# Optimization experiments

Measured on AMD Instinct MI355X. Metric: run time of the kernel, lower is better.

## Reference

```python
import jax, jax.numpy as jnp
import numpy as np
from jax import lax

N_LAYER = 24
N_EMBD = 1024
FFN = 4 * N_EMBD
LN_EPS = 1e-5


def setup_inputs() -> dict:
    key = jax.random.key(0)
    ks = jax.random.split(key, 24)
    L, C, F = N_LAYER, N_EMBD, FFN
    s = C ** -0.5  # keep GEMV outputs O(1) so exp() stays finite

    def rn(k, shape, scale=1.0):
        return jax.random.normal(k, shape, dtype=jnp.float32) * scale

    state = jnp.concatenate([
        rn(ks[1], (1, L, C)),                                          # statea: prev ln1 output
        rn(ks[2], (1, L, C), 0.1),                                     # stateb: wkv numerator acc
        jax.random.uniform(ks[3], (1, L, C), dtype=jnp.float32) + 0.5, # statec: wkv denominator acc (>0)
        rn(ks[4], (1, L, C)),                                          # stated: prev ln2 output
    ], axis=0)

    return {
        "x": rn(ks[0], (C,)),
        "state": state,
        "ln1w": 1.0 + rn(ks[5], (L, C), 0.02),
        "ln1b": rn(ks[6], (L, C), 0.02),
        "ln2w": 1.0 + rn(ks[7], (L, C), 0.02),
        "ln2b": rn(ks[8], (L, C), 0.02),
        "time_decay": -jnp.abs(rn(ks[9], (L, C))) - 0.1,
        "time_first": rn(ks[10], (L, C), 0.1),
        "kktk": jax.random.uniform(ks[11], (L, C), dtype=jnp.float32),
        "vvtv": jax.random.uniform(ks[12], (L, C), dtype=jnp.float32),
        "rrtr": jax.random.uniform(ks[13], (L, C), dtype=jnp.float32),
        "key": rn(ks[14], (L, 3, C, C), s),        # [kk, vv, -rr] stacks
        "outputv": rn(ks[15], (L, C, C), s),
        "time_mix_k_ffn": jax.random.uniform(ks[16], (L, C), dtype=jnp.float32),
        "time_mix_r_ffn": jax.random.uniform(ks[17], (L, C), dtype=jnp.float32),
        "key_ffn": rn(ks[18], (L, F, C), s),
        "receptance_ffn": rn(ks[19], (L, C, C), s),  # stored pre-negated, as in the module
        "value_ffn": rn(ks[20], (L, C, F), F ** -0.5),
    }


def _ln(v, w, b):
    m = v.mean()
    var = ((v - m) ** 2).mean()
    return (v - m) * lax.rsqrt(var + LN_EPS) * w + b


def reference(x, state, ln1w, ln1b, ln2w, ln2b, time_decay, time_first,
              kktk, vvtv, rrtr, key, outputv, time_mix_k_ffn, time_mix_r_ffn,
              key_ffn, receptance_ffn, value_ffn):
    # offset = 0, so the state slice covers all layers
    statea, stateb, statec, stated = state[0], state[1], state[2], state[3]  # each [L, C]
    # token-shift contributions precomputed against previous-step state
    kk_s = kktk * statea
    vv_s = vvtv * statea
    rr_s = rrtr * statea
    tmk_s = time_mix_k_ffn * stated
    tmr_s = time_mix_r_ffn * stated

    def layer(xc, p):
        (l1w, l1b, l2w, l2b, td, tfst, kks, vvs, rrs, keym, outv,
         tmk, tmr, kffn, rffn, vffn, sb, sc) = p
        xy = _ln(xc, l1w, l1b)
        k = keym[0] @ (xy + kks)
        v = keym[1] @ (xy + vvs)
        r = keym[2] @ (xy + rrs)   # keym[2] holds -receptance weights
        etfk = jnp.exp(tfst + k)
        w = (sb + etfk * v) / (sc * jnp.exp(r) + jnp.exp(tfst + k + r) + sc + etfk)
        sxx = xc + outv @ w
        ek = jnp.exp(k)
        ed = jnp.exp(td)
        sb_new = sb * ed + ek * v
        sc_new = sc * ed + ek
        xx = _ln(sxx, l2w, l2b)
        kf = jnp.square(jax.nn.relu(kffn @ (xx + tmk)))
        rf = jnp.exp(rffn @ (xx + tmr))  # rffn already negated
        x_new = sxx + (vffn @ kf) / (rf + 1.0)
        return x_new, (xy, sb_new, sc_new, xx)

    xs = (ln1w, ln1b, ln2w, ln2b, time_decay, time_first, kk_s, vv_s, rr_s,
          key, outputv, tmk_s, tmr_s, key_ffn, receptance_ffn, value_ffn,
          stateb, statec)
    x_out, (sa_n, sb_n, sc_n, sd_n) = lax.scan(layer, x, xs)
    new_state = jnp.stack([sa_n, sb_n, sc_n, sd_n])  # [4, L, C]
    return x_out, new_state
```

## Files before the change

### kernel.cpp

```cpp
#include <hip/hip_runtime.h>
#include <math.h>
#include <stddef.h>

#define NLAYER 24
#define NEMBD  1024
#define NFFN   4096
#define NB     256
#define NT     256
#define LN_EPS 1e-5f

#define OUT_SA (NEMBD)
#define OUT_SB (NEMBD + NLAYER*NEMBD)
#define OUT_SC (NEMBD + 2*NLAYER*NEMBD)
#define OUT_SD (NEMBD + 3*NLAYER*NEMBD)

typedef unsigned long long u64;
typedef unsigned u32;

#define QX_OFF    0
#define QKVR_OFF  1024
#define QSXX_OFF  4096
#define QKFB_OFF  5120
#define QTOTAL    9216

struct Params {
  const float *x, *state, *ln1w, *ln1b, *ln2w, *ln2b, *td, *tf, *kktk, *vvtv, *rrtr;
  const float *key, *outputv, *tmk, *tmr, *kffn, *rffn, *vffn;
  float *out;
  u64 *q;
};

__device__ __forceinline__ float wred(float v) {
#pragma unroll
  for (int o = 32; o > 0; o >>= 1) v += __shfl_xor(v, o, 64);
  return v;
}
__device__ __forceinline__ float dot4(float4 a, float4 b) {
  return a.x*b.x + a.y*b.y + a.z*b.z + a.w*b.w;
}
__device__ __forceinline__ float fcomp(float4 v, int j) {
  return j == 0 ? v.x : (j == 1 ? v.y : (j == 2 ? v.z : v.w));
}
__device__ __forceinline__ u64 qload(const u64* a) {
  return __hip_atomic_load(a, __ATOMIC_RELAXED, __HIP_MEMORY_SCOPE_AGENT);
}
__device__ __forceinline__ void qput(u64* a, float v, u32 tag) {
  u64 w = ((u64)tag << 32) | (u64)__float_as_uint(v);
  __hip_atomic_store(a, w, __ATOMIC_RELAXED, __HIP_MEMORY_SCOPE_AGENT);
}
__device__ __forceinline__ u32   qtag(u64 w) { return (u32)(w >> 32); }
__device__ __forceinline__ float qval(u64 w) { return __uint_as_float((u32)w); }

__device__ __forceinline__ void lbar() {
  asm volatile("s_waitcnt lgkmcnt(0)" ::: "memory");
  __builtin_amdgcn_s_barrier();
  asm volatile("" ::: "memory");
}

__global__ void __launch_bounds__(NT, 1)
rwkv_persistent(Params p) {
  const int b    = blockIdx.x;
  const int t    = threadIdx.x;
  const int wid  = t >> 6;
  const int lane = t & 63;
  const int i0   = t * 4;
  const int rowq = b * 4 + wid;

  __shared__ float lds[NFFN];
  __shared__ float part[8];
  __shared__ float sxw[4];
  __shared__ float rfw[4];

  u64* QX   = p.q + QX_OFF;
  u64* QKVR = p.q + QKVR_OFF;
  u64* QSXX = p.q + QSXX_OFF;
  u64* QKFB = p.q + QKFB_OFF;

  float4 wr[20];

  auto pf1 = [&](int L) {
    const float* W = p.key + (size_t)L * 3 * NEMBD * NEMBD
                   + (size_t)(b * 12 + wid * 3) * NEMBD + lane * 4;
#pragma unroll
    for (int r = 0; r < 3; ++r)
#pragma unroll
      for (int jj = 0; jj < 4; ++jj)
        wr[r * 4 + jj] = *(const float4*)&W[(size_t)r * NEMBD + jj * 256];
  };
  auto pf2 = [&](int L) {
    const float* W = p.outputv + ((size_t)L * NEMBD + rowq) * NEMBD + lane * 4;
#pragma unroll
    for (int jj = 0; jj < 4; ++jj)
      wr[jj] = *(const float4*)&W[jj * 256];
  };
  int isk3[5], rid3[5], voff3[5];
#pragma unroll
  for (int sI = 0; sI < 5; ++sI) {
    int qI = wid * 5 + sI;
    if (qI < 16) { isk3[sI] = 1; rid3[sI] = b * 16 + qI;       voff3[sI] = 0; }
    else         { isk3[sI] = 0; rid3[sI] = b * 4 + (qI - 16); voff3[sI] = NEMBD; }
  }
  auto pf3 = [&](int L) {
#pragma unroll
    for (int sI = 0; sI < 5; ++sI) {
      const float* wp = isk3[sI]
        ? p.kffn + ((size_t)L * NFFN  + rid3[sI]) * NEMBD
        : p.rffn + ((size_t)L * NEMBD + rid3[sI]) * NEMBD;
      wp += lane * 4;
#pragma unroll
      for (int jj = 0; jj < 4; ++jj)
        wr[sI * 4 + jj] = *(const float4*)&wp[jj * 256];
    }
  };
  auto pf4 = [&](int L) {
    const float* W = p.vffn + ((size_t)L * NEMBD + rowq) * NFFN + lane * 4;
#pragma unroll
    for (int jj = 0; jj < 16; ++jj)
      wr[jj] = *(const float4*)&W[jj * 256];
  };

  pf1(0);

  for (int l = 0; l < NLAYER; ++l) {
    const u32 t1 = (u32)(4 * l + 1), t2 = t1 + 1, t3 = t1 + 2, t4 = t1 + 3;
    const bool w1 = (b == (l * 4 + 0) % NB);
    const bool w2 = (b == (l * 4 + 1) % NB);
    const bool w3 = (b == (l * 4 + 2) % NB);

    {
      float xa[4];
      if (l == 0) {
        float4 x4 = *(const float4*)&p.x[i0];
        xa[0] = x4.x; xa[1] = x4.y; xa[2] = x4.z; xa[3] = x4.w;
      } else {
        const u32 tp = (u32)(4 * l);
        u64 a0, a1, a2, a3; long c = 0;
        for (;;) {
          a0 = qload(&QX[i0 + 0]); a1 = qload(&QX[i0 + 1]);
          a2 = qload(&QX[i0 + 2]); a3 = qload(&QX[i0 + 3]);
          if (qtag(a0) >= tp && qtag(a1) >= tp && qtag(a2) >= tp && qtag(a3) >= tp) break;
          __builtin_amdgcn_s_sleep(1);
          if (++c > (1L << 20)) break;
        }
        xa[0] = qval(a0); xa[1] = qval(a1); xa[2] = qval(a2); xa[3] = qval(a3);
      }
      float s = xa[0] + xa[1] + xa[2] + xa[3];
      float q = xa[0]*xa[0] + xa[1]*xa[1] + xa[2]*xa[2] + xa[3]*xa[3];
      s = wred(s); q = wred(q);
      if (lane == 0) { part[wid] = s; part[4 + wid] = q; }
      lbar();
      float m  = (part[0] + part[1] + part[2] + part[3]) * (1.f / NEMBD);
      float tq = (part[4] + part[5] + part[6] + part[7]) * (1.f / NEMBD);
      float rs = rsqrtf(tq - m * m + LN_EPS);
      const int o = l * NEMBD + i0;
      float4 l1w = *(const float4*)&p.ln1w[o];
      float4 l1b = *(const float4*)&p.ln1b[o];
      float4 sa  = *(const float4*)&p.state[0 * NLAYER * NEMBD + o];
      float4 kk  = *(const float4*)&p.kktk[o];
      float4 vv  = *(const float4*)&p.vvtv[o];
      float4 rr  = *(const float4*)&p.rrtr[o];
#pragma unroll
      for (int j = 0; j < 4; ++j) {
        int i = i0 + j;
        float xy  = (xa[j] - m) * rs * fcomp(l1w, j) + fcomp(l1b, j);
        float sav = fcomp(sa, j);
        lds[i]             = xy + fcomp(kk, j) * sav;
        lds[NEMBD + i]     = xy + fcomp(vv, j) * sav;
        lds[2 * NEMBD + i] = xy + fcomp(rr, j) * sav;
        if (w1) p.out[OUT_SA + l * NEMBD + i] = xy;
      }
      lbar();
      const int r0 = b * 12 + wid * 3;
      const float* v0 = lds + ((r0 + 0) >> 10) * NEMBD;
      const float* v1 = lds + ((r0 + 1) >> 10) * NEMBD;
      const float* v2 = lds + ((r0 + 2) >> 10) * NEMBD;
      float a0 = 0.f, a1 = 0.f, a2 = 0.f;
#pragma unroll
      for (int jj = 0; jj < 4; ++jj) {
        int col = lane * 4 + jj * 256;
        a0 += dot4(wr[0 * 4 + jj], *(const float4*)&v0[col]);
        a1 += dot4(wr[1 * 4 + jj], *(const float4*)&v1[col]);
        a2 += dot4(wr[2 * 4 + jj], *(const float4*)&v2[col]);
      }
      a0 = wred(a0); a1 = wred(a1); a2 = wred(a2);
      if (lane == 0) {
        qput(&QKVR[r0 + 0], a0, t1);
        qput(&QKVR[r0 + 1], a1, t1);
        qput(&QKVR[r0 + 2], a2, t1);
      }
      pf2(l);
      lbar();
    }

    {
      float kk[4], vv[4], rv[4];
      {
        u64 wk[4], wv[4], wq[4]; long c = 0;
        for (;;) {
          bool ok = true;
#pragma unroll
          for (int j = 0; j < 4; ++j) {
            wk[j] = qload(&QKVR[i0 + j]);
            wv[j] = qload(&QKVR[NEMBD + i0 + j]);
            wq[j] = qload(&QKVR[2 * NEMBD + i0 + j]);
            ok &= (qtag(wk[j]) >= t1) & (qtag(wv[j]) >= t1) & (qtag(wq[j]) >= t1);
          }
          if (ok) break;
          __builtin_amdgcn_s_sleep(1);
          if (++c > (1L << 20)) break;
        }
#pragma unroll
        for (int j = 0; j < 4; ++j) { kk[j] = qval(wk[j]); vv[j] = qval(wv[j]); rv[j] = qval(wq[j]); }
      }
      float xc;
      if (l == 0) xc = p.x[rowq];
      else {
        const u32 tp = (u32)(4 * l);
        u64 wx; long c = 0;
        for (;;) {
          wx = qload(&QX[rowq]);
          if (qtag(wx) >= tp) break;
          __builtin_amdgcn_s_sleep(1);
          if (++c > (1L << 20)) break;
        }
        xc = qval(wx);
      }
      const int o = l * NEMBD + i0;
      float4 tf = *(const float4*)&p.tf[o];
      float4 sb4 = *(const float4*)&p.state[1 * NLAYER * NEMBD + o];
      float4 sc4 = *(const float4*)&p.state[2 * NLAYER * NEMBD + o];
      float4 td4 = *(const float4*)&p.td[o];
#pragma unroll
      for (int j = 0; j < 4; ++j) {
        float sb = fcomp(sb4, j), sc = fcomp(sc4, j);
        float etfk = expf(fcomp(tf, j) + kk[j]);
        float er   = expf(rv[j]);
        lds[i0 + j] = (sb + etfk * vv[j]) / ((sc + etfk) * (1.f + er));
        if (w2) {
          float ek = expf(kk[j]), ed = expf(fcomp(td4, j));
          p.out[OUT_SB + l * NEMBD + i0 + j] = sb * ed + ek * vv[j];
          p.out[OUT_SC + l * NEMBD + i0 + j] = sc * ed + ek;
        }
      }
      lbar();
      float acc = 0.f;
#pragma unroll
      for (int jj = 0; jj < 4; ++jj) {
        int col = lane * 4 + jj * 256;
        acc += dot4(wr[jj], *(const float4*)&lds[col]);
      }
      acc = wred(acc);
      if (lane == 0) {
        float sxx = xc + acc;
        qput(&QSXX[rowq], sxx, t2);
        sxw[wid] = sxx;
      }
      pf3(l);
      lbar();
    }

    {
      float xa[4];
      {
        u64 a0, a1, a2, a3; long c = 0;
        for (;;) {
          a0 = qload(&QSXX[i0 + 0]); a1 = qload(&QSXX[i0 + 1]);
          a2 = qload(&QSXX[i0 + 2]); a3 = qload(&QSXX[i0 + 3]);
          if (qtag(a0) >= t2 && qtag(a1) >= t2 && qtag(a2) >= t2 && qtag(a3) >= t2) break;
          __builtin_amdgcn_s_sleep(1);
          if (++c > (1L << 20)) break;
        }
        xa[0] = qval(a0); xa[1] = qval(a1); xa[2] = qval(a2); xa[3] = qval(a3);
      }
      float s = xa[0] + xa[1] + xa[2] + xa[3];
      float q = xa[0]*xa[0] + xa[1]*xa[1] + xa[2]*xa[2] + xa[3]*xa[3];
      s = wred(s); q = wred(q);
      if (lane == 0) { part[wid] = s; part[4 + wid] = q; }
      lbar();
      float m  = (part[0] + part[1] + part[2] + part[3]) * (1.f / NEMBD);
      float tq = (part[4] + part[5] + part[6] + part[7]) * (1.f / NEMBD);
      float rs = rsqrtf(tq - m * m + LN_EPS);
      const int o = l * NEMBD + i0;
      float4 l2w = *(const float4*)&p.ln2w[o];
      float4 l2b = *(const float4*)&p.ln2b[o];
      float4 sd4 = *(const float4*)&p.state[3 * NLAYER * NEMBD + o];
      float4 tmk = *(const float4*)&p.tmk[o];
      float4 tmr = *(const float4*)&p.tmr[o];
#pragma unroll
      for (int j = 0; j < 4; ++j) {
        int i = i0 + j;
        float xx  = (xa[j] - m) * rs * fcomp(l2w, j) + fcomp(l2b, j);
        float sdv = fcomp(sd4, j);
        lds[i]         = xx + fcomp(tmk, j) * sdv;
        lds[NEMBD + i] = xx + fcomp(tmr, j) * sdv;
        if (w3) p.out[OUT_SD + l * NEMBD + i] = xx;
      }
      lbar();
      float acc[5] = {0.f, 0.f, 0.f, 0.f, 0.f};
#pragma unroll
      for (int jj = 0; jj < 4; ++jj) {
        int col = lane * 4 + jj * 256;
#pragma unroll
        for (int sI = 0; sI < 5; ++sI)
          acc[sI] += dot4(wr[sI * 4 + jj], *(const float4*)&lds[voff3[sI] + col]);
      }
#pragma unroll
      for (int sI = 0; sI < 5; ++sI) {
        float r = wred(acc[sI]);
        if (lane == 0) {
          if (isk3[sI]) { float kv = fmaxf(r, 0.f); qput(&QKFB[rid3[sI]], kv * kv, t3); }
          else          { rfw[rid3[sI] - b * 4] = expf(r); }
        }
      }
      pf4(l);
      lbar();
    }

    {
      {
        u64 w[16]; long c = 0;
        for (;;) {
          bool ok = true;
#pragma unroll
          for (int pass = 0; pass < 4; ++pass)
#pragma unroll
            for (int j = 0; j < 4; ++j) {
              w[pass * 4 + j] = qload(&QKFB[pass * NEMBD + i0 + j]);
              ok &= (qtag(w[pass * 4 + j]) >= t3);
            }
          if (ok) break;
          __builtin_amdgcn_s_sleep(1);
          if (++c > (1L << 20)) break;
        }
#pragma unroll
        for (int pass = 0; pass < 4; ++pass)
#pragma unroll
          for (int j = 0; j < 4; ++j)
            lds[pass * NEMBD + i0 + j] = qval(w[pass * 4 + j]);
      }
      lbar();
      float accA = 0.f, accB = 0.f;
#pragma unroll
      for (int jj = 0; jj < 16; jj += 2) {
        int col = lane * 4 + jj * 256;
        accA += dot4(wr[jj],     *(const float4*)&lds[col]);
        accB += dot4(wr[jj + 1], *(const float4*)&lds[col + 256]);
      }
      float acc = wred(accA + accB);
      if (lane == 0) {
        float xn = sxw[wid] + acc / (rfw[wid] + 1.f);
        if (l == NLAYER - 1) p.out[rowq] = xn;
        else                 qput(&QX[rowq], xn, t4);
      }
      if (l < NLAYER - 1) pf1(l + 1);
      lbar();
    }
  }
}

__global__ void rwkv_init(u64* q) {
  for (int i = 0; i < 36; ++i)
    q[threadIdx.x * 36 + i] = 0ull;
}

extern "C" void kernel_launch(void* const* d_in, const int* in_sizes, int n_in,
                              void* d_out, int out_size, void* d_ws, size_t ws_size,
                              hipStream_t stream) {
  Params p;
  p.x       = (const float*)d_in[0];
  p.state   = (const float*)d_in[1];
  p.ln1w    = (const float*)d_in[2];
  p.ln1b    = (const float*)d_in[3];
  p.ln2w    = (const float*)d_in[4];
  p.ln2b    = (const float*)d_in[5];
  p.td      = (const float*)d_in[6];
  p.tf      = (const float*)d_in[7];
  p.kktk    = (const float*)d_in[8];
  p.vvtv    = (const float*)d_in[9];
  p.rrtr    = (const float*)d_in[10];
  p.key     = (const float*)d_in[11];
  p.outputv = (const float*)d_in[12];
  p.tmk     = (const float*)d_in[13];
  p.tmr     = (const float*)d_in[14];
  p.kffn    = (const float*)d_in[15];
  p.rffn    = (const float*)d_in[16];
  p.vffn    = (const float*)d_in[17];
  p.out     = (float*)d_out;
  p.q       = (u64*)d_ws;

  rwkv_init<<<1, NB, 0, stream>>>(p.q);
  rwkv_persistent<<<NB, NT, 0, stream>>>(p);
}
```

Baseline: 449.4 us.

## Dedicate one wave to polling and split GEMV work across three compute waves

Wave 0 now does all cross-block polling of the tagged queues with coalesced per-lane loads and __all, staging the results into LDS. Waves 1-3 only compute the GEMV rows, which are redistributed among them: four rows each for KVR, split outputv rows, seven FFN rows each, and a column split of value_ffn with an LDS partial-sum reduction. Per-layer parameter vectors and weights for the next stage are prefetched into registers earlier, so polling latency can overlap with loads. In exchange, register use rises (wA[28]+wB[24]), the work split across the three compute waves is uneven, and an extra barrier is added for the final reduction.

```diff
diff --git a/kernel.cpp b/kernel.cpp
--- a/kernel.cpp
+++ b/kernel.cpp
@@ -23,6 +23,15 @@
 #define QKFB_OFF  5120
 #define QTOTAL    9216
 
+#define LACT 0
+#define LMSK 4096
+#define LLN  7168
+#define LXL  7176
+#define LSXL 7180
+#define LRFL 7184
+#define LPT  7188
+#define SMTOT 7200
+
 struct Params {
   const float *x, *state, *ln1w, *ln1b, *ln2w, *ln2b, *td, *tf, *kktk, *vvtv, *rrtr;
   const float *key, *outputv, *tmk, *tmr, *kffn, *rffn, *vffn;
@@ -56,6 +65,23 @@
   __builtin_amdgcn_s_barrier();
   asm volatile("" ::: "memory");
 }
+
+#define POLLN(N, QBASE, TG, LOFF)                                              \
+  do {                                                                         \
+    u64 pw_[N]; long cc_ = 0;                                                  \
+    for (;;) {                                                                 \
+      bool ok_ = true;                                                         \
+      _Pragma("unroll")                                                        \
+      for (int c_ = 0; c_ < N; ++c_) pw_[c_] = qload((QBASE) + c_*64 + lane);  \
+      _Pragma("unroll")                                                        \
+      for (int c_ = 0; c_ < N; ++c_) ok_ &= (qtag(pw_[c_]) >= (TG));           \
+      if (__all(ok_)) break;                                                   \
+      __builtin_amdgcn_s_sleep(1);                                             \
+      if (++cc_ > (1L << 20)) break;             \
+    }                                                                          \
+    _Pragma("unroll")                                                          \
+    for (int c_ = 0; c_ < N; ++c_) sm[(LOFF) + c_*64 + lane] = qval(pw_[c_]);  \
+  } while (0)
 
 __global__ void __launch_bounds__(NT, 1)
 rwkv_persistent(Params p) {
@@ -64,62 +90,93 @@
   const int wid  = t >> 6;
   const int lane = t & 63;
   const int i0   = t * 4;
-  const int rowq = b * 4 + wid;
-
-  __shared__ float lds[NFFN];
-  __shared__ float part[8];
-  __shared__ float sxw[4];
-  __shared__ float rfw[4];
+  const bool w0  = (wid == 0);
+  const int cw   = wid - 1;
+
+  __shared__ float sm[SMTOT];
 
   u64* QX   = p.q + QX_OFF;
   u64* QKVR = p.q + QKVR_OFF;
   u64* QSXX = p.q + QSXX_OFF;
   u64* QKFB = p.q + QKFB_OFF;
 
-  float4 wr[20];
-
-  auto pf1 = [&](int L) {
+  float4 wA[28], wB[24];
+  float4 prA[6], prB[4];
+
+  auto params1 = [&](int L) {
+    const int o = L * NEMBD + i0;
+    prA[0] = *(const float4*)&p.ln1w[o];
+    prA[1] = *(const float4*)&p.ln1b[o];
+    prA[2] = *(const float4*)&p.state[0 * NLAYER * NEMBD + o];
+    prA[3] = *(const float4*)&p.kktk[o];
+    prA[4] = *(const float4*)&p.vvtv[o];
+    prA[5] = *(const float4*)&p.rrtr[o];
+  };
+  auto params2 = [&](int L) {
+    const int o = L * NEMBD + i0;
+    prB[0] = *(const float4*)&p.tf[o];
+    prB[1] = *(const float4*)&p.state[1 * NLAYER * NEMBD + o];
+    prB[2] = *(const float4*)&p.state[2 * NLAYER * NEMBD + o];
+    prB[3] = *(const float4*)&p.td[o];
+  };
+  auto params3 = [&](int L) {
+    const int o = L * NEMBD + i0;
+    prA[0] = *(const float4*)&p.ln2w[o];
+    prA[1] = *(const float4*)&p.ln2b[o];
+    prA[2] = *(const float4*)&p.state[3 * NLAYER * NEMBD + o];
+    prA[3] = *(const float4*)&p.tmk[o];
+    prA[4] = *(const float4*)&p.tmr[o];
+  };
+  auto weights1 = [&](int L) {
     const float* W = p.key + (size_t)L * 3 * NEMBD * NEMBD
-                   + (size_t)(b * 12 + wid * 3) * NEMBD + lane * 4;
-#pragma unroll
-    for (int r = 0; r < 3; ++r)
+                   + (size_t)(b * 12 + cw * 4) * NEMBD + lane * 4;
+#pragma unroll
+    for (int q = 0; q < 4; ++q)
 #pragma unroll
       for (int jj = 0; jj < 4; ++jj)
-        wr[r * 4 + jj] = *(const float4*)&W[(size_t)r * NEMBD + jj * 256];
-  };
-  auto pf2 = [&](int L) {
-    const float* W = p.outputv + ((size_t)L * NEMBD + rowq) * NEMBD + lane * 4;
-#pragma unroll
-    for (int jj = 0; jj < 4; ++jj)
-      wr[jj] = *(const float4*)&W[jj * 256];
-  };
-  int isk3[5], rid3[5], voff3[5];
-#pragma unroll
-  for (int sI = 0; sI < 5; ++sI) {
-    int qI = wid * 5 + sI;
-    if (qI < 16) { isk3[sI] = 1; rid3[sI] = b * 16 + qI;       voff3[sI] = 0; }
-    else         { isk3[sI] = 0; rid3[sI] = b * 4 + (qI - 16); voff3[sI] = NEMBD; }
-  }
-  auto pf3 = [&](int L) {
-#pragma unroll
-    for (int sI = 0; sI < 5; ++sI) {
-      const float* wp = isk3[sI]
-        ? p.kffn + ((size_t)L * NFFN  + rid3[sI]) * NEMBD
-        : p.rffn + ((size_t)L * NEMBD + rid3[sI]) * NEMBD;
-      wp += lane * 4;
-#pragma unroll
-      for (int jj = 0; jj < 4; ++jj)
-        wr[sI * 4 + jj] = *(const float4*)&wp[jj * 256];
-    }
-  };
-  auto pf4 = [&](int L) {
-    const float* W = p.vffn + ((size_t)L * NEMBD + rowq) * NFFN + lane * 4;
-#pragma unroll
-    for (int jj = 0; jj < 16; ++jj)
-      wr[jj] = *(const float4*)&W[jj * 256];
-  };
-
-  pf1(0);
+        wA[q * 4 + jj] = *(const float4*)&W[(size_t)q * NEMBD + jj * 256];
+  };
+  auto weights2 = [&](int L) {
+#pragma unroll
+    for (int rr = 0; rr < 2; ++rr) {
+      if (cw == 0 || rr == 0) {
+        const int r = (cw == 0) ? rr : (cw + 1);
+        const float* W = p.outputv + ((size_t)L * NEMBD + b * 4 + r) * NEMBD + lane * 4;
+#pragma unroll
+        for (int jj = 0; jj < 4; ++jj)
+          wB[rr * 4 + jj] = *(const float4*)&W[jj * 256];
+      }
+    }
+  };
+  auto weights3 = [&](int L) {
+#pragma unroll
+    for (int e = 0; e < 7; ++e) {
+      const int sidx = cw * 7 + e;
+      if (sidx < 20) {
+        const float* W = (sidx < 16)
+          ? p.kffn + ((size_t)L * NFFN  + b * 16 + sidx) * NEMBD
+          : p.rffn + ((size_t)L * NEMBD + b * 4 + (sidx - 16)) * NEMBD;
+        W += lane * 4;
+#pragma unroll
+        for (int jj = 0; jj < 4; ++jj)
+          wA[e * 4 + jj] = *(const float4*)&W[jj * 256];
+      }
+    }
+  };
+  auto weights4 = [&](int L) {
+    const int jb = (cw == 0) ? 0 : ((cw == 1) ? 6 : 11);
+    const int jn = (cw == 0) ? 6 : 5;
+#pragma unroll
+    for (int r = 0; r < 4; ++r) {
+      const float* W = p.vffn + ((size_t)L * NEMBD + b * 4 + r) * NFFN + lane * 4;
+#pragma unroll
+      for (int c = 0; c < 6; ++c) if (c < jn)
+        wB[r * 6 + c] = *(const float4*)&W[(jb + c) * 256];
+    }
+  };
+
+  params1(0); params2(0);
+  if (!w0) { weights1(0); weights2(0); }
 
   for (int l = 0; l < NLAYER; ++l) {
     const u32 t1 = (u32)(4 * l + 1), t2 = t1 + 1, t3 = t1 + 2, t4 = t1 + 3;
@@ -128,232 +185,174 @@
     const bool w3 = (b == (l * 4 + 2) % NB);
 
     {
+      if (w0) {
+        if (l == 0) {
+#pragma unroll
+          for (int c = 0; c < 16; ++c)
+            sm[LACT + c * 64 + lane] = p.x[c * 64 + lane];
+        } else {
+          POLLN(16, QX, (u32)(4 * l), LACT);
+        }
+      }
+      lbar();
       float xa[4];
-      if (l == 0) {
-        float4 x4 = *(const float4*)&p.x[i0];
-        xa[0] = x4.x; xa[1] = x4.y; xa[2] = x4.z; xa[3] = x4.w;
-      } else {
-        const u32 tp = (u32)(4 * l);
-        u64 a0, a1, a2, a3; long c = 0;
-        for (;;) {
-          a0 = qload(&QX[i0 + 0]); a1 = qload(&QX[i0 + 1]);
-          a2 = qload(&QX[i0 + 2]); a3 = qload(&QX[i0 + 3]);
-          if (qtag(a0) >= tp && qtag(a1) >= tp && qtag(a2) >= tp && qtag(a3) >= tp) break;
-          __builtin_amdgcn_s_sleep(1);
-          if (++c > (1L << 20)) break;
-        }
-        xa[0] = qval(a0); xa[1] = qval(a1); xa[2] = qval(a2); xa[3] = qval(a3);
-      }
+#pragma unroll
+      for (int j = 0; j < 4; ++j) xa[j] = sm[LACT + i0 + j];
       float s = xa[0] + xa[1] + xa[2] + xa[3];
       float q = xa[0]*xa[0] + xa[1]*xa[1] + xa[2]*xa[2] + xa[3]*xa[3];
       s = wred(s); q = wred(q);
-      if (lane == 0) { part[wid] = s; part[4 + wid] = q; }
-      lbar();
-      float m  = (part[0] + part[1] + part[2] + part[3]) * (1.f / NEMBD);
-      float tq = (part[4] + part[5] + part[6] + part[7]) * (1.f / NEMBD);
+      if (lane == 0) { sm[LLN + wid] = s; sm[LLN + 4 + wid] = q; }
+      lbar();
+      float m  = (sm[LLN+0] + sm[LLN+1] + sm[LLN+2] + sm[LLN+3]) * (1.f / NEMBD);
+      float tq = (sm[LLN+4] + sm[LLN+5] + sm[LLN+6] + sm[LLN+7]) * (1.f / NEMBD);
       float rs = rsqrtf(tq - m * m + LN_EPS);
-      const int o = l * NEMBD + i0;
-      float4 l1w = *(const float4*)&p.ln1w[o];
-      float4 l1b = *(const float4*)&p.ln1b[o];
-      float4 sa  = *(const float4*)&p.state[0 * NLAYER * NEMBD + o];
-      float4 kk  = *(const float4*)&p.kktk[o];
-      float4 vv  = *(const float4*)&p.vvtv[o];
-      float4 rr  = *(const float4*)&p.rrtr[o];
 #pragma unroll
       for (int j = 0; j < 4; ++j) {
         int i = i0 + j;
-        float xy  = (xa[j] - m) * rs * fcomp(l1w, j) + fcomp(l1b, j);
-        float sav = fcomp(sa, j);
-        lds[i]             = xy + fcomp(kk, j) * sav;
-        lds[NEMBD + i]     = xy + fcomp(vv, j) * sav;
-        lds[2 * NEMBD + i] = xy + fcomp(rr, j) * sav;
+        float xy  = (xa[j] - m) * rs * fcomp(prA[0], j) + fcomp(prA[1], j);
+        float sav = fcomp(prA[2], j);
+        sm[LMSK + i]        = xy + fcomp(prA[3], j) * sav;
+        sm[LMSK + 1024 + i] = xy + fcomp(prA[4], j) * sav;
+        sm[LMSK + 2048 + i] = xy + fcomp(prA[5], j) * sav;
         if (w1) p.out[OUT_SA + l * NEMBD + i] = xy;
       }
-      lbar();
-      const int r0 = b * 12 + wid * 3;
-      const float* v0 = lds + ((r0 + 0) >> 10) * NEMBD;
-      const float* v1 = lds + ((r0 + 1) >> 10) * NEMBD;
-      const float* v2 = lds + ((r0 + 2) >> 10) * NEMBD;
-      float a0 = 0.f, a1 = 0.f, a2 = 0.f;
-#pragma unroll
-      for (int jj = 0; jj < 4; ++jj) {
-        int col = lane * 4 + jj * 256;
-        a0 += dot4(wr[0 * 4 + jj], *(const float4*)&v0[col]);
-        a1 += dot4(wr[1 * 4 + jj], *(const float4*)&v1[col]);
-        a2 += dot4(wr[2 * 4 + jj], *(const float4*)&v2[col]);
-      }
-      a0 = wred(a0); a1 = wred(a1); a2 = wred(a2);
-      if (lane == 0) {
-        qput(&QKVR[r0 + 0], a0, t1);
-        qput(&QKVR[r0 + 1], a1, t1);
-        qput(&QKVR[r0 + 2], a2, t1);
-      }
-      pf2(l);
-      lbar();
+      if (t < 4) sm[LXL + t] = sm[LACT + b * 4 + t];
+      lbar();
+      if (!w0) {
+        const int r0 = b * 12 + cw * 4;
+#pragma unroll
+        for (int qq = 0; qq < 4; ++qq) {
+          const float* mv = &sm[LMSK + ((r0 + qq) >> 10) * 1024];
+          float a = 0.f;
+#pragma unroll
+          for (int jj = 0; jj < 4; ++jj)
+            a += dot4(wA[qq * 4 + jj], *(const float4*)&mv[lane * 4 + jj * 256]);
+          a = wred(a);
+          if (lane == 0) qput(&QKVR[r0 + qq], a, t1);
+        }
+        params3(l); weights3(l);
+      } else {
+        params3(l);
+      }
     }
 
     {
+      if (w0) POLLN(48, QKVR, t1, LACT);
+      lbar();
       float kk[4], vv[4], rv[4];
-      {
-        u64 wk[4], wv[4], wq[4]; long c = 0;
-        for (;;) {
-          bool ok = true;
-#pragma unroll
-          for (int j = 0; j < 4; ++j) {
-            wk[j] = qload(&QKVR[i0 + j]);
-            wv[j] = qload(&QKVR[NEMBD + i0 + j]);
-            wq[j] = qload(&QKVR[2 * NEMBD + i0 + j]);
-            ok &= (qtag(wk[j]) >= t1) & (qtag(wv[j]) >= t1) & (qtag(wq[j]) >= t1);
-          }
-          if (ok) break;
-          __builtin_amdgcn_s_sleep(1);
-          if (++c > (1L << 20)) break;
-        }
-#pragma unroll
-        for (int j = 0; j < 4; ++j) { kk[j] = qval(wk[j]); vv[j] = qval(wv[j]); rv[j] = qval(wq[j]); }
-      }
-      float xc;
-      if (l == 0) xc = p.x[rowq];
-      else {
-        const u32 tp = (u32)(4 * l);
-        u64 wx; long c = 0;
-        for (;;) {
-          wx = qload(&QX[rowq]);
-          if (qtag(wx) >= tp) break;
-          __builtin_amdgcn_s_sleep(1);
-          if (++c > (1L << 20)) break;
-        }
-        xc = qval(wx);
-      }
-      const int o = l * NEMBD + i0;
-      float4 tf = *(const float4*)&p.tf[o];
-      float4 sb4 = *(const float4*)&p.state[1 * NLAYER * NEMBD + o];
-      float4 sc4 = *(const float4*)&p.state[2 * NLAYER * NEMBD + o];
-      float4 td4 = *(const float4*)&p.td[o];
 #pragma unroll
       for (int j = 0; j < 4; ++j) {
-        float sb = fcomp(sb4, j), sc = fcomp(sc4, j);
-        float etfk = expf(fcomp(tf, j) + kk[j]);
+        kk[j] = sm[LACT + i0 + j];
+        vv[j] = sm[LACT + 1024 + i0 + j];
+        rv[j] = sm[LACT + 2048 + i0 + j];
+      }
+#pragma unroll
+      for (int j = 0; j < 4; ++j) {
+        float sb = fcomp(prB[1], j), sc = fcomp(prB[2], j);
+        float etfk = expf(fcomp(prB[0], j) + kk[j]);
         float er   = expf(rv[j]);
-        lds[i0 + j] = (sb + etfk * vv[j]) / ((sc + etfk) * (1.f + er));
+        sm[LMSK + i0 + j] = (sb + etfk * vv[j]) / ((sc + etfk) * (1.f + er));
         if (w2) {
-          float ek = expf(kk[j]), ed = expf(fcomp(td4, j));
+          float ek = expf(kk[j]), ed = expf(fcomp(prB[3], j));
           p.out[OUT_SB + l * NEMBD + i0 + j] = sb * ed + ek * vv[j];
           p.out[OUT_SC + l * NEMBD + i0 + j] = sc * ed + ek;
         }
       }
       lbar();
-      float acc = 0.f;
-#pragma unroll
-      for (int jj = 0; jj < 4; ++jj) {
-        int col = lane * 4 + jj * 256;
-        acc += dot4(wr[jj], *(const float4*)&lds[col]);
-      }
-      acc = wred(acc);
-      if (lane == 0) {
-        float sxx = xc + acc;
-        qput(&QSXX[rowq], sxx, t2);
-        sxw[wid] = sxx;
-      }
-      pf3(l);
-      lbar();
+      if (!w0) {
+#pragma unroll
+        for (int rr = 0; rr < 2; ++rr) {
+          if (cw == 0 || rr == 0) {
+            const int r = (cw == 0) ? rr : (cw + 1);
+            float a = 0.f;
+#pragma unroll
+            for (int jj = 0; jj < 4; ++jj)
+              a += dot4(wB[rr * 4 + jj], *(const float4*)&sm[LMSK + lane * 4 + jj * 256]);
+            a = wred(a);
+            if (lane == 0) {
+              float sxx = sm[LXL + r] + a;
+              qput(&QSXX[b * 4 + r], sxx, t2);
+              sm[LSXL + r] = sxx;
+            }
+          }
+        }
+        weights4(l);
+      }
     }
 
     {
+      if (w0) POLLN(16, QSXX, t2, LACT);
+      lbar();
       float xa[4];
-      {
-        u64 a0, a1, a2, a3; long c = 0;
-        for (;;) {
-          a0 = qload(&QSXX[i0 + 0]); a1 = qload(&QSXX[i0 + 1]);
-          a2 = qload(&QSXX[i0 + 2]); a3 = qload(&QSXX[i0 + 3]);
-          if (qtag(a0) >= t2 && qtag(a1) >= t2 && qtag(a2) >= t2 && qtag(a3) >= t2) break;
-          __builtin_amdgcn_s_sleep(1);
-          if (++c > (1L << 20)) break;
-        }
-        xa[0] = qval(a0); xa[1] = qval(a1); xa[2] = qval(a2); xa[3] = qval(a3);
-      }
+#pragma unroll
+      for (int j = 0; j < 4; ++j) xa[j] = sm[LACT + i0 + j];
       float s = xa[0] + xa[1] + xa[2] + xa[3];
       float q = xa[0]*xa[0] + xa[1]*xa[1] + xa[2]*xa[2] + xa[3]*xa[3];
       s = wred(s); q = wred(q);
-      if (lane == 0) { part[wid] = s; part[4 + wid] = q; }
-      lbar();
-      float m  = (part[0] + part[1] + part[2] + part[3]) * (1.f / NEMBD);
-      float tq = (part[4] + part[5] + part[6] + part[7]) * (1.f / NEMBD);
+      if (lane == 0) { sm[LLN + wid] = s; sm[LLN + 4 + wid] = q; }
+      lbar();
+      float m  = (sm[LLN+0] + sm[LLN+1] + sm[LLN+2] + sm[LLN+3]) * (1.f / NEMBD);
+      float tq = (sm[LLN+4] + sm[LLN+5] + sm[LLN+6] + sm[LLN+7]) * (1.f / NEMBD);
       float rs = rsqrtf(tq - m * m + LN_EPS);
-      const int o = l * NEMBD + i0;
-      float4 l2w = *(const float4*)&p.ln2w[o];
-      float4 l2b = *(const float4*)&p.ln2b[o];
-      float4 sd4 = *(const float4*)&p.state[3 * NLAYER * NEMBD + o];
-      float4 tmk = *(const float4*)&p.tmk[o];
-      float4 tmr = *(const float4*)&p.tmr[o];
 #pragma unroll
       for (int j = 0; j < 4; ++j) {
         int i = i0 + j;
-        float xx  = (xa[j] - m) * rs * fcomp(l2w, j) + fcomp(l2b, j);
-        float sdv = fcomp(sd4, j);
-        lds[i]         = xx + fcomp(tmk, j) * sdv;
-        lds[NEMBD + i] = xx + fcomp(tmr, j) * sdv;
+        float xx  = (xa[j] - m) * rs * fcomp(prA[0], j) + fcomp(prA[1], j);
+        float sdv = fcomp(prA[2], j);
+        sm[LMSK + i]        = xx + fcomp(prA[3], j) * sdv;
+        sm[LMSK + 1024 + i] = xx + fcomp(prA[4], j) * sdv;
         if (w3) p.out[OUT_SD + l * NEMBD + i] = xx;
       }
       lbar();
-      float acc[5] = {0.f, 0.f, 0.f, 0.f, 0.f};
-#pragma unroll
-      for (int jj = 0; jj < 4; ++jj) {
-        int col = lane * 4 + jj * 256;
-#pragma unroll
-        for (int sI = 0; sI < 5; ++sI)
-          acc[sI] += dot4(wr[sI * 4 + jj], *(const float4*)&lds[voff3[sI] + col]);
-      }
-#pragma unroll
-      for (int sI = 0; sI < 5; ++sI) {
-        float r = wred(acc[sI]);
-        if (lane == 0) {
-          if (isk3[sI]) { float kv = fmaxf(r, 0.f); qput(&QKFB[rid3[sI]], kv * kv, t3); }
-          else          { rfw[rid3[sI] - b * 4] = expf(r); }
-        }
-      }
-      pf4(l);
-      lbar();
+      if (!w0) {
+#pragma unroll
+        for (int e = 0; e < 7; ++e) {
+          const int sidx = cw * 7 + e;
+          if (sidx < 20) {
+            const float* mv = &sm[LMSK + ((sidx < 16) ? 0 : 1024)];
+            float a = 0.f;
+#pragma unroll
+            for (int jj = 0; jj < 4; ++jj)
+              a += dot4(wA[e * 4 + jj], *(const float4*)&mv[lane * 4 + jj * 256]);
+            a = wred(a);
+            if (lane == 0) {
+              if (sidx < 16) { float kv = fmaxf(a, 0.f); qput(&QKFB[b * 16 + sidx], kv * kv, t3); }
+              else           { sm[LRFL + (sidx - 16)] = expf(a); }
+            }
+          }
+        }
+        if (l + 1 < NLAYER) { params1(l + 1); weights1(l + 1); }
+      } else {
+        if (l + 1 < NLAYER) params1(l + 1);
+      }
     }
 
     {
-      {
-        u64 w[16]; long c = 0;
-        for (;;) {
-          bool ok = true;
-#pragma unroll
-          for (int pass = 0; pass < 4; ++pass)
-#pragma unroll
-            for (int j = 0; j < 4; ++j) {
-              w[pass * 4 + j] = qload(&QKFB[pass * NEMBD + i0 + j]);
-              ok &= (qtag(w[pass * 4 + j]) >= t3);
-            }
-          if (ok) break;
-          __builtin_amdgcn_s_sleep(1);
-          if (++c > (1L << 20)) break;
-        }
-#pragma unroll
-        for (int pass = 0; pass < 4; ++pass)
-#pragma unroll
-          for (int j = 0; j < 4; ++j)
-            lds[pass * NEMBD + i0 + j] = qval(w[pass * 4 + j]);
-      }
-      lbar();
-      float accA = 0.f, accB = 0.f;
-#pragma unroll
-      for (int jj = 0; jj < 16; jj += 2) {
-        int col = lane * 4 + jj * 256;
-        accA += dot4(wr[jj],     *(const float4*)&lds[col]);
-        accB += dot4(wr[jj + 1], *(const float4*)&lds[col + 256]);
-      }
-      float acc = wred(accA + accB);
-      if (lane == 0) {
-        float xn = sxw[wid] + acc / (rfw[wid] + 1.f);
-        if (l == NLAYER - 1) p.out[rowq] = xn;
-        else                 qput(&QX[rowq], xn, t4);
-      }
-      if (l < NLAYER - 1) pf1(l + 1);
-      lbar();
+      if (w0) POLLN(64, QKFB, t3, LACT);
+      lbar();
+      if (!w0) {
+        const int jb = (cw == 0) ? 0 : ((cw == 1) ? 6 : 11);
+        const int jn = (cw == 0) ? 6 : 5;
+#pragma unroll
+        for (int r = 0; r < 4; ++r) {
+          float a = 0.f;
+#pragma unroll
+          for (int c = 0; c < 6; ++c) if (c < jn)
+            a += dot4(wB[r * 6 + c], *(const float4*)&sm[LACT + lane * 4 + (jb + c) * 256]);
+          a = wred(a);
+          if (lane == 0) sm[LPT + r * 3 + cw] = a;
+        }
+        if (l + 1 < NLAYER) { params2(l + 1); weights2(l + 1); }
+      } else {
+        if (l + 1 < NLAYER) params2(l + 1);
+      }
+      lbar();
+      if (w0 && lane < 4) {
+        float tot = sm[LPT + lane * 3] + sm[LPT + lane * 3 + 1] + sm[LPT + lane * 3 + 2];
+        float xn  = sm[LSXL + lane] + tot / (sm[LRFL + lane] + 1.f);
+        if (l == NLAYER - 1) p.out[b * 4 + lane] = xn;
+        else                 qput(&QX[b * 4 + lane], xn, t4);
+      }
     }
   }
 }
```

Result: slower. 1.531 ms (+240.7%).
